# Optimization experiments

Measured on AMD Instinct MI355X. Metric: run time of the kernel, lower is better.

Reference implementation:

```python
import jax, jax.numpy as jnp
import numpy as np

D_MODEL, N_LEVELS, N_HEADS, N_POINTS = 256, 4, 8, 4
SHAPES = [(100, 100), (50, 50), (25, 25), (13, 13)]  # (H, W) per level


def setup_inputs() -> dict:
    key = jax.random.key(0)
    ks = jax.random.split(key, 8)
    N = 2
    C = D_MODEL
    Len_in = sum(h * w for h, w in SHAPES)
    Lq = Len_in  # encoder self-attention
    query = jax.random.normal(ks[0], (N, Lq, C), jnp.float32)
    reference_points = jax.random.uniform(ks[1], (N, Lq, N_LEVELS, 2), dtype=jnp.float32)
    input_flatten = jax.random.normal(ks[2], (N, Len_in, C), jnp.float32)
    input_spatial_shapes = np.array(SHAPES, dtype=np.int64)
    areas = input_spatial_shapes[:, 0] * input_spatial_shapes[:, 1]
    input_level_start_index = np.concatenate([[0], np.cumsum(areas)[:-1]]).astype(np.int64)
    s = 1.0 / np.sqrt(C)
    Wv = jax.random.uniform(ks[3], (C, C), jnp.float32, -s, s)
    bv = jnp.zeros((C,), jnp.float32)
    # sampling_offsets: small random weight + the module's grid bias init
    Woff = jax.random.normal(ks[4], (N_HEADS * N_LEVELS * N_POINTS * 2, C), jnp.float32) * 0.01
    thetas = jnp.arange(N_HEADS, dtype=jnp.float32) * (2.0 * np.pi / N_HEADS)
    grid = jnp.stack([jnp.cos(thetas), jnp.sin(thetas)], -1)  # (M,2)
    grid = grid / jnp.max(jnp.abs(grid), axis=-1, keepdims=True)
    grid = jnp.tile(grid[:, None, None, :], (1, N_LEVELS, N_POINTS, 1))
    grid = grid * (jnp.arange(N_POINTS, dtype=jnp.float32) + 1.0)[None, None, :, None]
    boff = grid.reshape(-1)
    Wa = jax.random.normal(ks[5], (N_HEADS * N_LEVELS * N_POINTS, C), jnp.float32) * 0.02
    ba = jnp.zeros((N_HEADS * N_LEVELS * N_POINTS,), jnp.float32)
    Wo = jax.random.uniform(ks[6], (C, C), jnp.float32, -s, s)
    bo = jnp.zeros((C,), jnp.float32)
    return {
        'query': query, 'reference_points': reference_points, 'input_flatten': input_flatten,
        'input_spatial_shapes': input_spatial_shapes, 'input_level_start_index': input_level_start_index,
        'Wv': Wv, 'bv': bv, 'Woff': Woff, 'boff': boff, 'Wa': Wa, 'ba': ba, 'Wo': Wo, 'bo': bo,
    }


def _msda_forward(query, reference_points, input_flatten, shapes, starts,
                  Wv, bv, Woff, boff, Wa, ba, Wo, bo):
    N, Lq, C = query.shape
    M, L, P = N_HEADS, N_LEVELS, N_POINTS
    D = C // M
    value = (input_flatten @ Wv.T + bv).reshape(N, -1, M, D)  # (N, Len_in, M, D)
    off = (query @ Woff.T + boff).reshape(N, Lq, M, L, P, 2)
    attn = jax.nn.softmax((query @ Wa.T + ba).reshape(N, Lq, M, L * P), axis=-1)
    attn = attn.reshape(N, Lq, M, L, P)
    # offset_normalizer = (W_l, H_l)
    norm = jnp.asarray(shapes[:, ::-1].copy(), jnp.float32)  # (L, 2)
    loc = reference_points[:, :, None, :, None, :] + off / norm[None, None, None, :, None, :]
    grids = 2.0 * loc - 1.0  # (N, Lq, M, L, P, 2), grid_sample convention
    out = jnp.zeros((N, Lq, M, D), query.dtype)
    for l in range(L):
        H, W = int(shapes[l, 0]), int(shapes[l, 1])
        s0 = int(starts[l])
        v = value[:, s0:s0 + H * W]  # (N, H*W, M, D)
        # align_corners=False unnormalization
        gx = ((grids[:, :, :, l, :, 0] + 1.0) * W - 1.0) / 2.0  # (N, Lq, M, P)
        gy = ((grids[:, :, :, l, :, 1] + 1.0) * H - 1.0) / 2.0
        x0 = jnp.floor(gx); y0 = jnp.floor(gy)
        fx = gx - x0;       fy = gy - y0
        x0i = x0.astype(jnp.int32); y0i = y0.astype(jnp.int32)

        def gather(iy, ix):
            valid = (iy >= 0) & (iy < H) & (ix >= 0) & (ix < W)
            lin = jnp.clip(iy, 0, H - 1) * W + jnp.clip(ix, 0, W - 1)  # (N, Lq, M, P)
            lin2 = lin.transpose(0, 1, 3, 2).reshape(N, Lq * P, M)
            g = jnp.take_along_axis(v, lin2[..., None], axis=1)  # (N, Lq*P, M, D)
            g = g.reshape(N, Lq, P, M, D).transpose(0, 1, 3, 2, 4)  # (N, Lq, M, P, D)
            return g * valid[..., None]  # zero padding outside

        s00 = gather(y0i, x0i)
        s01 = gather(y0i, x0i + 1)
        s10 = gather(y0i + 1, x0i)
        s11 = gather(y0i + 1, x0i + 1)
        sampled = (s00 * ((1 - fy) * (1 - fx))[..., None] + s01 * ((1 - fy) * fx)[..., None]
                   + s10 * (fy * (1 - fx))[..., None] + s11 * (fy * fx)[..., None])
        out = out + jnp.einsum('nqmp,nqmpd->nqmd', attn[:, :, :, l], sampled)
    out = out.reshape(N, Lq, C)
    return out @ Wo.T + bo


def reference(query, reference_points, input_flatten, input_spatial_shapes, input_level_start_index,
              Wv, bv, Woff, boff, Wa, ba, Wo, bo):
    shapes = np.asarray(input_spatial_shapes)
    starts = np.asarray(input_level_start_index)
    return _msda_forward(query, reference_points, input_flatten, shapes, starts,
                         Wv, bv, Woff, boff, Wa, ba, Wo, bo)
```

## Files before the change

kernel.cpp:

```cpp
#include <hip/hip_runtime.h>
#include <math.h>

#define NB   2
#define LQ   13294
#define NROWS (NB*LQ)
#define CDIM 256
#define HSLICES (NROWS + 1)
#define HS32 ((size_t)HSLICES * 32)

typedef unsigned short u16;
typedef unsigned int   u32;
typedef short bf16x8 __attribute__((ext_vector_type(8)));
typedef float f32x4  __attribute__((ext_vector_type(4)));
typedef float f32x2  __attribute__((ext_vector_type(2)));

struct alignas(8) U16x4 { u16 x, y, z, w; };

__device__ __forceinline__ u16 f2bf(float f) {
    u32 u = __builtin_bit_cast(u32, f);
    u += 0x7FFFu + ((u >> 16) & 1u);
    return (u16)(u >> 16);
}

__device__ __forceinline__ void gload_lds16(const void* g, void* l) {
    __builtin_amdgcn_global_load_lds(
        (__attribute__((address_space(1))) void*)g,
        (__attribute__((address_space(3))) void*)l, 16, 0, 0);
}

__device__ __forceinline__ f32x2 bfpair(u32 u) {
    union { u32 w[2]; f32x2 v; } x;
    x.w[0] = u << 16;
    x.w[1] = u & 0xFFFF0000u;
    return x.v;
}

__global__ __launch_bounds__(256)
void prep_all(const float4* __restrict__ query, const float4* __restrict__ inflat,
              const float* __restrict__ Wv, const float* __restrict__ Woff,
              const float* __restrict__ Wa, const float* __restrict__ Wo,
              u16* __restrict__ qb, u16* __restrict__ ib,
              u16* __restrict__ wb) {
    const int b = blockIdx.x;
    const int t = threadIdx.x;
    if (b < 6647) {
        int i = b * 256 + t;
        float4 v = query[i];
        U16x4 o{f2bf(v.x), f2bf(v.y), f2bf(v.z), f2bf(v.w)};
        *(U16x4*)&qb[(size_t)i * 4] = o;
    } else if (b < 13294) {
        int i = (b - 6647) * 256 + t;
        float4 v = inflat[i];
        U16x4 o{f2bf(v.x), f2bf(v.y), f2bf(v.z), f2bf(v.w)};
        *(U16x4*)&ib[(size_t)i * 4] = o;
    } else {
        int i = (b - 13294) * 256 + t;
        float v;
        if      (i <  65536) v = Wv[i];
        else if (i < 131072) v = Woff[i - 65536];
        else if (i < 163840) v = Wa[i - 131072];
        else                 v = Wo[i - 163840];
        wb[i] = f2bf(v);
    }
}

__device__ __forceinline__ void gemm_core64(
    const u16* __restrict__ A, const u16* __restrict__ Bw, int M, int row0,
    u16* As, u16* Bs, f32x4 (&acc)[2][4]) {
    const int tid  = threadIdx.x;
    const int lane = tid & 63;
    const int wave = tid >> 6;
    const int ln16 = lane & 15;
    const int kq   = lane >> 4;
    const int wr   = (wave >> 1) * 32;
    const int wc   = (wave & 1) * 64;

    #pragma unroll
    for (int kt = 0; kt < 4; ++kt) {
        const int k0 = kt * 64;
        #pragma unroll
        for (int it = 0; it < 2; ++it) {
            int chunk = it * 256 + tid;
            int row = chunk >> 3, ch = chunk & 7;
            int chs = (ch ^ (row & 7)) * 8;
            int gra = min(row0 + row, M - 1);
            gload_lds16(A + (size_t)gra * 256 + k0 + chs, As + chunk * 8);
        }
        #pragma unroll
        for (int it = 0; it < 4; ++it) {
            int cb = it * 256 + tid;
            int row = cb >> 3, ch = cb & 7;
            int chs = (ch ^ (row & 7)) * 8;
            gload_lds16(Bw + (size_t)row * 256 + k0 + chs, Bs + cb * 8);
        }
        __syncthreads();
        #pragma unroll
        for (int kf = 0; kf < 2; ++kf) {
            const int ck = kf * 4 + kq;
            bf16x8 a[2], b[4];
            #pragma unroll
            for (int i = 0; i < 2; ++i) {
                int r = wr + i * 16 + ln16;
                a[i] = *(const bf16x8*)&As[r * 64 + ((ck ^ (r & 7)) * 8)];
            }
            #pragma unroll
            for (int j = 0; j < 4; ++j) {
                int c = wc + j * 16 + ln16;
                b[j] = *(const bf16x8*)&Bs[c * 64 + ((ck ^ (c & 7)) * 8)];
            }
            #pragma unroll
            for (int i = 0; i < 2; ++i)
                #pragma unroll
                for (int j = 0; j < 4; ++j)
                    acc[i][j] = __builtin_amdgcn_mfma_f32_16x16x32_bf16(
                        a[i], b[j], acc[i][j], 0, 0, 0);
        }
        __syncthreads();
    }
}

__global__ __launch_bounds__(256, 4)
void gemm_front(const u16* __restrict__ qb, const u16* __restrict__ ib,
                const u16* __restrict__ wb, const float* __restrict__ bv,
                const float* __restrict__ boff, const float* __restrict__ ba,
                u16* __restrict__ value, float* __restrict__ offb,
                float* __restrict__ logit, int M) {
    __shared__ u16 Sh[64 * 64 + 128 * 64];
    u16* As = Sh;
    u16* Bs = Sh + 4096;
    const int s    = blockIdx.x;
    const int row0 = blockIdx.y * 64;
    const u16* A  = (s < 2) ? ib : qb;
    const u16* Bw = wb + (size_t)s * 32768;
    const float* bias = (s == 0) ? bv
                      : (s == 1) ? bv + 128
                      : (s == 2) ? boff
                      : (s == 3) ? boff + 128
                      : ba;

    f32x4 acc[2][4] = {};
    gemm_core64(A, Bw, M, row0, As, Bs, acc);

    const int tid  = threadIdx.x;
    const int lane = tid & 63;
    const int wave = tid >> 6;
    const int ln16 = lane & 15, kq = lane >> 4;
    const int wr = (wave >> 1) * 32, wc = (wave & 1) * 64;

    if (s < 2) {
        #pragma unroll
        for (int j = 0; j < 4; ++j) {
            int cl = wc + j * 16 + ln16;
            float bj = bias[cl];
            #pragma unroll
            for (int i = 0; i < 2; ++i)
                #pragma unroll
                for (int r = 0; r < 4; ++r) {
                    int rl = wr + i * 16 + kq * 4 + r;
                    Sh[rl * 128 + cl] = f2bf(acc[i][j][r] + bj);
                }
        }
        __syncthreads();
        #pragma unroll
        for (int it = 0; it < 4; ++it) {
            int ci = it * 256 + tid;
            int tr = ci >> 4;
            int cc = ci & 15;
            int gr = row0 + tr;
            if (gr < M) {
                int cg = s * 128 + cc * 8;
                u16* dst = value + (size_t)(cg >> 5) * HS32
                                 + (size_t)gr * 32 + (cg & 31);
                *(uint4*)dst = *(const uint4*)&Sh[tr * 128 + cc * 8];
            }
        }
        if (s == 0 && blockIdx.y == 0) {
            value[(size_t)(tid >> 5) * HS32 + (size_t)NROWS * 32 + (tid & 31)] = 0;
        }
    } else {
        #pragma unroll
        for (int j = 0; j < 4; ++j) {
            int lc = wc + j * 16 + ln16;
            float bj = bias[lc];
            #pragma unroll
            for (int i = 0; i < 2; ++i) {
                #pragma unroll
                for (int r = 0; r < 4; ++r) {
                    int gr = row0 + wr + i * 16 + kq * 4 + r;
                    if (gr < M) {
                        float o = acc[i][j][r] + bj;
                        if (s < 4)
                            offb[(size_t)gr * 256 + (s - 2) * 128 + lc] = o;
                        else
                            logit[(size_t)gr * 128 + lc] = o;
                    }
                }
            }
        }
    }
}

__global__ __launch_bounds__(256, 4)
void gemm_out(const u16* __restrict__ A, const u16* __restrict__ Bw0,
              const float* __restrict__ bias, float* __restrict__ C, int M) {
    __shared__ u16 Sh[64 * 64 + 128 * 64];
    u16* As = Sh;
    u16* Bs = Sh + 4096;
    const int s    = blockIdx.x;
    const int row0 = blockIdx.y * 64;
    const u16* Bw = Bw0 + (size_t)s * 32768;

    f32x4 acc[2][4] = {};
    gemm_core64(A, Bw, M, row0, As, Bs, acc);

    const int lane = threadIdx.x & 63;
    const int wave = threadIdx.x >> 6;
    const int ln16 = lane & 15, kq = lane >> 4;
    const int wr = (wave >> 1) * 32, wc = (wave & 1) * 64;
    #pragma unroll
    for (int j = 0; j < 4; ++j) {
        int gc = s * 128 + wc + j * 16 + ln16;
        float bj = bias[gc];
        #pragma unroll
        for (int i = 0; i < 2; ++i) {
            #pragma unroll
            for (int r = 0; r < 4; ++r) {
                int gr = row0 + wr + i * 16 + kq * 4 + r;
                if (gr < M) C[(size_t)gr * 256 + gc] = acc[i][j][r] + bj;
            }
        }
    }
}

__global__ __launch_bounds__(256, 4)
void msda_sample(const u16* __restrict__ value,
                 const float* __restrict__ refpts,
                 const float* __restrict__ off,
                 const float* __restrict__ logits,
                 u16* __restrict__ tmp) {
    __shared__ float sAw[4][8][16];
    __shared__ int   sLin[4][8][17][2];
    __shared__ float sW[4][8][17][4];

    const int t  = threadIdx.x;
    const int qb = blockIdx.x * 4;

    if (t < 32) {
        const int qi = t >> 3, m = t & 7;
        const float* lg = logits + (size_t)(qb + qi) * 128 + m * 16;
        float e[16];
        float mx = -1e30f;
        #pragma unroll
        for (int i = 0; i < 16; ++i) { e[i] = lg[i]; mx = fmaxf(mx, e[i]); }
        float s = 0.f;
        #pragma unroll
        for (int i = 0; i < 16; ++i) { e[i] = __expf(e[i] - mx); s += e[i]; }
        const float inv = 1.f / s;
        #pragma unroll
        for (int i = 0; i < 16; ++i) sAw[qi][m][i] = e[i] * inv;
    }
    __syncthreads();

    #pragma unroll
    for (int j2 = 0; j2 < 2; ++j2) {
        const int job = t + j2 * 256;
        const int qi = job >> 7;
        const int m  = (job >> 4) & 7;
        const int p  = job & 15;
        const int l  = p >> 2, pp = p & 3;
        const int q  = qb + qi;
        const int n  = (q >= LQ) ? 1 : 0;

        const int W = (l == 0) ? 100 : (l == 1) ? 50 : (l == 2) ? 25 : 13;
        const int H = W;
        const int st = (l == 0) ? 0 : (l == 1) ? 10000 : (l == 2) ? 12500 : 13125;
        const float invW = (l == 0) ? 0.01f : (l == 1) ? 0.02f
                         : (l == 2) ? 0.04f : (1.f / 13.f);

        const float rx = refpts[(size_t)q * 8 + l * 2 + 0];
        const float ry = refpts[(size_t)q * 8 + l * 2 + 1];
        const float ox = off[(size_t)q * 256 + m * 32 + (l * 4 + pp) * 2 + 0];
        const float oy = off[(size_t)q * 256 + m * 32 + (l * 4 + pp) * 2 + 1];

        const float locx = rx + ox * invW;
        const float locy = ry + oy * invW;
        const float grx = 2.f * locx - 1.f;
        const float gry = 2.f * locy - 1.f;
        const float gx = ((grx + 1.f) * (float)W - 1.f) * 0.5f;
        const float gy = ((gry + 1.f) * (float)H - 1.f) * 0.5f;
        const float x0f = floorf(gx), y0f = floorf(gy);
        const float fx = gx - x0f, fy = gy - y0f;
        const int x0 = (int)x0f, y0 = (int)y0f;
        const int x1 = x0 + 1, y1 = y0 + 1;

        const int cx0 = min(max(x0, 0), W - 1);
        const int cy0 = min(max(y0, 0), H - 1);
        const int cy1 = min(max(y1, 0), H - 1);
        const bool vx0 = (x0 >= 0) & (x0 < W);
        const bool vx1 = (x1 >= 0) & (x1 < W);
        const bool vy0 = (y0 >= 0) & (y0 < H);
        const bool vy1 = (y1 >= 0) & (y1 < H);

        const float aw = sAw[qi][m][p];
        const int base = n * LQ + st;
        const float w00 = (vy0 & vx0) ? aw * (1.f - fy) * (1.f - fx) : 0.f;
        const float w01 = (vy0 & vx1) ? aw * (1.f - fy) * fx         : 0.f;
        const float w10 = (vy1 & vx0) ? aw * fy * (1.f - fx)         : 0.f;
        const float w11 = (vy1 & vx1) ? aw * fy * fx                 : 0.f;
        const bool fold = (x0 < 0);
        sLin[qi][m][p][0] = base + cy0 * W + cx0;
        sLin[qi][m][p][1] = base + cy1 * W + cx0;
        sW[qi][m][p][0] = fold ? w01 : w00;
        sW[qi][m][p][1] = fold ? 0.f : w01;
        sW[qi][m][p][2] = fold ? w11 : w10;
        sW[qi][m][p][3] = fold ? 0.f : w11;
    }
    __syncthreads();

    const int qi = t >> 6;
    const int m  = (t >> 3) & 7;
    const int e  = t & 7;
    const int xh = e >> 2;
    const int c4 = e & 3;
    const int q  = qb + qi;
    const char* vb = (const char*)value + (size_t)m * (HS32 * 2);
    const u32 eoff = (u32)e * 16u;

    f32x2 a2[4] = {{0.f, 0.f}, {0.f, 0.f}, {0.f, 0.f}, {0.f, 0.f}};

    int2   rbA = *(const int2*)  &sLin[qi][m][0][0];
    float4 w4A = *(const float4*)&sW  [qi][m][0][0];
    uint4  rA0 = *(const uint4*)(vb + ((u32)rbA.x * 64u + eoff));
    uint4  rA1 = *(const uint4*)(vb + ((u32)rbA.y * 64u + eoff));

    #pragma unroll
    for (int p = 0; p < 16; ++p) {
        int2   rbB; float4 w4B; uint4 rB0, rB1;
        if (p < 15) {
            rbB = *(const int2*)  &sLin[qi][m][p + 1][0];
            w4B = *(const float4*)&sW  [qi][m][p + 1][0];
            rB0 = *(const uint4*)(vb + ((u32)rbB.x * 64u + eoff));
            rB1 = *(const uint4*)(vb + ((u32)rbB.y * 64u + eoff));
        } else {
            rbB = rbA; w4B = w4A; rB0 = rA0; rB1 = rA1;
        }
        const float wa  = xh ? w4A.y : w4A.x;
        const float wb_ = xh ? w4A.w : w4A.z;
        f32x2 wa2 = {wa, wa};
        f32x2 wb2 = {wb_, wb_};
        a2[0] += wa2 * bfpair(rA0.x); a2[1] += wa2 * bfpair(rA0.y);
        a2[2] += wa2 * bfpair(rA0.z); a2[3] += wa2 * bfpair(rA0.w);
        a2[0] += wb2 * bfpair(rA1.x); a2[1] += wb2 * bfpair(rA1.y);
        a2[2] += wb2 * bfpair(rA1.z); a2[3] += wb2 * bfpair(rA1.w);
        rbA = rbB; w4A = w4B; rA0 = rB0; rA1 = rB1;
    }
    #pragma unroll
    for (int k = 0; k < 4; ++k) {
        a2[k].x += __shfl_xor(a2[k].x, 4);
        a2[k].y += __shfl_xor(a2[k].y, 4);
    }
    if (xh == 0) {
        uint4 o;
        o.x = (u32)f2bf(a2[0].x) | ((u32)f2bf(a2[0].y) << 16);
        o.y = (u32)f2bf(a2[1].x) | ((u32)f2bf(a2[1].y) << 16);
        o.z = (u32)f2bf(a2[2].x) | ((u32)f2bf(a2[2].y) << 16);
        o.w = (u32)f2bf(a2[3].x) | ((u32)f2bf(a2[3].y) << 16);
        *(uint4*)((char*)tmp + ((u32)q * 512u + (u32)m * 64u + (u32)c4 * 16u)) = o;
    }
}

extern "C" void kernel_launch(void* const* d_in, const int* in_sizes, int n_in,
                              void* d_out, int out_size, void* d_ws, size_t ws_size,
                              hipStream_t stream) {
    const float* query  = (const float*)d_in[0];
    const float* refpts = (const float*)d_in[1];
    const float* inflat = (const float*)d_in[2];
    const float* Wv   = (const float*)d_in[5];
    const float* bv   = (const float*)d_in[6];
    const float* Woff = (const float*)d_in[7];
    const float* boff = (const float*)d_in[8];
    const float* Wa   = (const float*)d_in[9];
    const float* ba   = (const float*)d_in[10];
    const float* Wo   = (const float*)d_in[11];
    const float* bo   = (const float*)d_in[12];
    float* out = (float*)d_out;

    char* ws = (char*)d_ws;
    constexpr size_t SZ16  = (size_t)NROWS * 256 * 2;
    constexpr size_t SZVAL = ((size_t)HSLICES * 512 + 4095) & ~(size_t)4095;
    constexpr size_t SZ32  = (size_t)NROWS * 256 * 4;
    constexpr size_t SZL   = (size_t)NROWS * 128 * 4;
    u16*   qb    = (u16*)(ws);
    u16*   ib    = (u16*)(ws + SZ16);
    u16*   value = (u16*)(ws + 2 * SZ16);
    float* offb  = (float*)(ws + 2 * SZ16 + SZVAL);
    float* logit = (float*)(ws + 2 * SZ16 + SZVAL + SZ32);
    u16*   wb    = (u16*)(ws + 2 * SZ16 + SZVAL + SZ32 + SZL);
    u16*   tmp   = qb;

    const int RG = (NROWS + 63) / 64;

    hipLaunchKernelGGL(prep_all, dim3(14190), dim3(256), 0, stream,
                       (const float4*)query, (const float4*)inflat,
                       Wv, Woff, Wa, Wo, qb, ib, wb);

    gemm_front<<<dim3(5, RG), dim3(256), 0, stream>>>(
        qb, ib, wb, bv, boff, ba, value, offb, logit, NROWS);

    hipLaunchKernelGGL(msda_sample, dim3(NROWS / 4), dim3(256), 0, stream,
                       value, refpts, offb, logit, tmp);

    gemm_out<<<dim3(2, RG), dim3(256), 0, stream>>>(
        tmp, wb + 163840, bo, out, NROWS);
}
```

Measured before the change: 203.8 us.

## Preload full weight tile into LDS and double-buffer A tiles in GEMMs

```diff
diff --git a/kernel.cpp b/kernel.cpp
--- a/kernel.cpp
+++ b/kernel.cpp
@@ -33,6 +33,12 @@
     x.w[0] = u << 16;
     x.w[1] = u & 0xFFFF0000u;
     return x.v;
+}
+
+__device__ __forceinline__ void block_barrier() {
+    asm volatile("" ::: "memory");
+    __builtin_amdgcn_s_barrier();
+    asm volatile("" ::: "memory");
 }
 
 __global__ __launch_bounds__(256)
@@ -64,9 +70,55 @@
     }
 }
 
-__device__ __forceinline__ void gemm_core64(
+template<int KT>
+__device__ __forceinline__ void kstep(
+    const u16* __restrict__ A, int M, int row0, int tid,
+    const u16* AsCur, u16* AsAlt, const u16* Bs,
+    int wr, int wc, int ln16, int kq, f32x4 (&acc)[2][4]) {
+    if constexpr (KT < 3) {
+        const int k0n = (KT + 1) * 64;
+        #pragma unroll
+        for (int it = 0; it < 2; ++it) {
+            int chunk = it * 256 + tid;
+            int row = chunk >> 3, ch = chunk & 7;
+            int chs = (ch ^ (row & 7)) * 8;
+            int gra = min(row0 + row, M - 1);
+            gload_lds16(A + (size_t)gra * 256 + k0n + chs, AsAlt + chunk * 8);
+        }
+        asm volatile("s_waitcnt vmcnt(2)" ::: "memory");
+    } else {
+        asm volatile("s_waitcnt vmcnt(0)" ::: "memory");
+    }
+    block_barrier();
+    #pragma unroll
+    for (int kf = 0; kf < 2; ++kf) {
+        const int ck = kf * 4 + kq;
+        const int gk = KT * 8 + ck;
+        bf16x8 a[2], b[4];
+        #pragma unroll
+        for (int i = 0; i < 2; ++i) {
+            int r = wr + i * 16 + ln16;
+            a[i] = *(const bf16x8*)&AsCur[r * 64 + ((ck ^ (r & 7)) * 8)];
+        }
+        #pragma unroll
+        for (int j = 0; j < 4; ++j) {
+            int c = wc + j * 16 + ln16;
+            int lch = (gk & 24) | ((gk & 7) ^ (c & 7));
+            b[j] = *(const bf16x8*)&Bs[c * 256 + lch * 8];
+        }
+        #pragma unroll
+        for (int i = 0; i < 2; ++i)
+            #pragma unroll
+            for (int j = 0; j < 4; ++j)
+                acc[i][j] = __builtin_amdgcn_mfma_f32_16x16x32_bf16(
+                    a[i], b[j], acc[i][j], 0, 0, 0);
+    }
+    block_barrier();
+}
+
+__device__ __forceinline__ void gemm_core_pipe(
     const u16* __restrict__ A, const u16* __restrict__ Bw, int M, int row0,
-    u16* As, u16* Bs, f32x4 (&acc)[2][4]) {
+    u16* Bs, u16* As0, u16* As1, f32x4 (&acc)[2][4]) {
     const int tid  = threadIdx.x;
     const int lane = tid & 63;
     const int wave = tid >> 6;
@@ -76,58 +128,39 @@
     const int wc   = (wave & 1) * 64;
 
     #pragma unroll
-    for (int kt = 0; kt < 4; ++kt) {
-        const int k0 = kt * 64;
-        #pragma unroll
-        for (int it = 0; it < 2; ++it) {
-            int chunk = it * 256 + tid;
-            int row = chunk >> 3, ch = chunk & 7;
-            int chs = (ch ^ (row & 7)) * 8;
-            int gra = min(row0 + row, M - 1);
-            gload_lds16(A + (size_t)gra * 256 + k0 + chs, As + chunk * 8);
-        }
-        #pragma unroll
-        for (int it = 0; it < 4; ++it) {
-            int cb = it * 256 + tid;
-            int row = cb >> 3, ch = cb & 7;
-            int chs = (ch ^ (row & 7)) * 8;
-            gload_lds16(Bw + (size_t)row * 256 + k0 + chs, Bs + cb * 8);
-        }
-        __syncthreads();
-        #pragma unroll
-        for (int kf = 0; kf < 2; ++kf) {
-            const int ck = kf * 4 + kq;
-            bf16x8 a[2], b[4];
-            #pragma unroll
-            for (int i = 0; i < 2; ++i) {
-                int r = wr + i * 16 + ln16;
-                a[i] = *(const bf16x8*)&As[r * 64 + ((ck ^ (r & 7)) * 8)];
-            }
-            #pragma unroll
-            for (int j = 0; j < 4; ++j) {
-                int c = wc + j * 16 + ln16;
-                b[j] = *(const bf16x8*)&Bs[c * 64 + ((ck ^ (c & 7)) * 8)];
-            }
-            #pragma unroll
-            for (int i = 0; i < 2; ++i)
-                #pragma unroll
-                for (int j = 0; j < 4; ++j)
-                    acc[i][j] = __builtin_amdgcn_mfma_f32_16x16x32_bf16(
-                        a[i], b[j], acc[i][j], 0, 0, 0);
-        }
-        __syncthreads();
-    }
-}
-
-__global__ __launch_bounds__(256, 4)
+    for (int it = 0; it < 16; ++it) {
+        int cb = it * 256 + tid;
+        int row = cb >> 5, ch = cb & 31;
+        int chs = (ch & 24) | ((ch & 7) ^ (row & 7));
+        gload_lds16(Bw + (size_t)row * 256 + chs * 8, Bs + cb * 8);
+    }
+    #pragma unroll
+    for (int it = 0; it < 2; ++it) {
+        int chunk = it * 256 + tid;
+        int row = chunk >> 3, ch = chunk & 7;
+        int chs = (ch ^ (row & 7)) * 8;
+        int gra = min(row0 + row, M - 1);
+        gload_lds16(A + (size_t)gra * 256 + chs, As0 + chunk * 8);
+    }
+    asm volatile("s_waitcnt vmcnt(0)" ::: "memory");
+    block_barrier();
+
+    kstep<0>(A, M, row0, tid, As0, As1, Bs, wr, wc, ln16, kq, acc);
+    kstep<1>(A, M, row0, tid, As1, As0, Bs, wr, wc, ln16, kq, acc);
+    kstep<2>(A, M, row0, tid, As0, As1, Bs, wr, wc, ln16, kq, acc);
+    kstep<3>(A, M, row0, tid, As1, As0, Bs, wr, wc, ln16, kq, acc);
+}
+
+__global__ __launch_bounds__(256, 2)
 void gemm_front(const u16* __restrict__ qb, const u16* __restrict__ ib,
                 const u16* __restrict__ wb, const float* __restrict__ bv,
                 const float* __restrict__ boff, const float* __restrict__ ba,
                 u16* __restrict__ value, float* __restrict__ offb,
                 float* __restrict__ logit, int M) {
-    __shared__ u16 Sh[64 * 64 + 128 * 64];
-    u16* As = Sh;
-    u16* Bs = Sh + 4096;
+    __shared__ u16 Sh[32768 + 8192];
+    u16* Bs  = Sh;
+    u16* As0 = Sh + 32768;
+    u16* As1 = Sh + 32768 + 4096;
     const int s    = blockIdx.x;
     const int row0 = blockIdx.y * 64;
     const u16* A  = (s < 2) ? ib : qb;
@@ -139,7 +172,7 @@
                       : ba;
 
     f32x4 acc[2][4] = {};
-    gemm_core64(A, Bw, M, row0, As, Bs, acc);
+    gemm_core_pipe(A, Bw, M, row0, Bs, As0, As1, acc);
 
     const int tid  = threadIdx.x;
     const int lane = tid & 63;
@@ -200,18 +233,19 @@
     }
 }
 
-__global__ __launch_bounds__(256, 4)
+__global__ __launch_bounds__(256, 2)
 void gemm_out(const u16* __restrict__ A, const u16* __restrict__ Bw0,
               const float* __restrict__ bias, float* __restrict__ C, int M) {
-    __shared__ u16 Sh[64 * 64 + 128 * 64];
-    u16* As = Sh;
-    u16* Bs = Sh + 4096;
+    __shared__ u16 Sh[32768 + 8192];
+    u16* Bs  = Sh;
+    u16* As0 = Sh + 32768;
+    u16* As1 = Sh + 32768 + 4096;
     const int s    = blockIdx.x;
     const int row0 = blockIdx.y * 64;
     const u16* Bw = Bw0 + (size_t)s * 32768;
 
     f32x4 acc[2][4] = {};
-    gemm_core64(A, Bw, M, row0, As, Bs, acc);
+    gemm_core_pipe(A, Bw, M, row0, Bs, As0, As1, acc);
 
     const int lane = threadIdx.x & 63;
     const int wave = threadIdx.x >> 6;
```

New measurement: 216.1 us. 1.06x slower.
